# Performance work log

Measured on AMD Instinct MI355X. Metric: run time of the kernel, lower is better.

The kernel has to match this reference:

```python
import jax, jax.numpy as jnp
import numpy as np

EPS = 1e-6  # torch.nn.PairwiseDistance default eps: dist = ||x - y + eps||_2


def setup_inputs() -> dict:
    key = jax.random.key(0)
    k1, k2 = jax.random.split(key)
    samples = jax.random.normal(k1, (4096, 128), dtype=jnp.float32)   # batch of observations
    V = jax.random.uniform(k2, (65536, 128), dtype=jnp.float32)       # grown node codebook (torch.rand init)
    return {"samples": samples, "V": V}


def reference(samples, V):
    # activate_bmu, vectorized over the batch.
    # torch PairwiseDistance(p=2): d_n = || x - V_n + eps ||_2
    D = samples.shape[-1]
    x_sq = jnp.sum(samples * samples, axis=-1)        # [B]
    v_sq = jnp.sum(V * V, axis=-1)                    # [N]
    xv = jnp.einsum('bd,nd->bn', samples, V)          # [B, N]
    x_sum = jnp.sum(samples, axis=-1)                 # [B]
    v_sum = jnp.sum(V, axis=-1)                       # [N]
    sq = (x_sq[:, None] + v_sq[None, :] - 2.0 * xv
          + 2.0 * EPS * (x_sum[:, None] - v_sum[None, :]) + D * EPS * EPS)
    dists = jnp.sqrt(jnp.maximum(sq, 0.0))            # [B, N]
    # top-2 smallest distances -> BMU b, second BMU s
    neg_top2, idx = jax.lax.top_k(-dists, 2)          # [B, 2]
    b = idx[:, 0]
    s = idx[:, 1]
    a = jnp.exp(neg_top2[:, 0])                       # exp(-b_dist)
    return (b, s, a)
```

## Files before the change

### kernel.cpp

```cpp
#include <hip/hip_runtime.h>
#include <math.h>

#define NS 4096
#define NV 65536
#define DDIM 128
#define EPSV 1e-6f
#define NCHUNK 16
#define TILES_PER_CHUNK 32
#define FLTMAX 3.402823466e+38f
#define IMAX 0x7fffffff

#define VSQ_F   0
#define VSUM_F  65536
#define XSQ_F   131072
#define XSUM_F  135168
#define PART_F  139264
#define WS_TILED_BYTE 1605632
#define TILE_BYTES 65536
#define TILE_STRIDE 66560

typedef __attribute__((ext_vector_type(8)))  __bf16        bf16x8;
typedef __attribute__((ext_vector_type(8)))  unsigned short ush8;
typedef __attribute__((ext_vector_type(4)))  unsigned short ush4;
typedef __attribute__((ext_vector_type(16))) float          f32x16;

typedef const __attribute__((address_space(1))) unsigned int* gp_t;
typedef __attribute__((address_space(3))) unsigned int*       lp_t;

__device__ __forceinline__ void async_cp16(const void* g, void* l) {
    __builtin_amdgcn_global_load_lds((gp_t)g, (lp_t)l, 16, 0, 0);
}

__device__ __forceinline__ unsigned short f2bf(float x) {
    unsigned u = __builtin_bit_cast(unsigned, x);
    u += 0x7FFFu + ((u >> 16) & 1u);
    return (unsigned short)(u >> 16);
}
__device__ __forceinline__ float bf2f(unsigned short h) {
    unsigned u = ((unsigned)h) << 16;
    return __builtin_bit_cast(float, u);
}

__device__ __forceinline__ void merge2t(float& d1, int& i1, float& d2, int& i2,
                                        float d, int i) {
    bool b1 = (d < d1) || (d == d1 && i < i1);
    bool b2 = (d < d2) || (d == d2 && i < i2);
    if (b1) { d2 = d1; i2 = i1; d1 = d; i1 = i; }
    else if (b2) { d2 = d; i2 = i; }
}

__global__ void vq_precompute(const float* __restrict__ samples,
                              const float* __restrict__ V,
                              float* __restrict__ ws) {
    const int wave = threadIdx.x >> 6;
    const int lane = threadIdx.x & 63;
    int row = blockIdx.x * 4 + wave;
    const float* src; float* sqo; float* sumo; int r;
    if (row < NV) {
        r = row; src = V + (size_t)r * DDIM; sqo = ws + VSQ_F; sumo = ws + VSUM_F;
    } else {
        r = row - NV;
        if (r >= NS) return;
        src = samples + (size_t)r * DDIM; sqo = ws + XSQ_F; sumo = ws + XSUM_F;
    }
    float2 v = ((const float2*)src)[lane];
    float s = v.x + v.y;
    float q = v.x * v.x + v.y * v.y;
    #pragma unroll
    for (int off = 32; off >= 1; off >>= 1) {
        s += __shfl_xor(s, off);
        q += __shfl_xor(q, off);
    }
    if (lane == 0) { sqo[r] = q; sumo[r] = s; }
}

__global__ void vq_cj(const float* __restrict__ ws_f, char* __restrict__ ws) {
    int c = blockIdx.x * 256 + threadIdx.x;
    float cj = ws_f[VSQ_F + c] - 2.0f * EPSV * ws_f[VSUM_F + c];
    int tile = c >> 7, m = c & 127;
    *(float*)(ws + WS_TILED_BYTE + (size_t)tile * TILE_STRIDE + TILE_BYTES + m * 4) = cj;
}

__global__ void vq_convertV(const float* __restrict__ V, char* __restrict__ ws) {
    const int tile = blockIdx.x;
    const int tid = threadIdx.x;
    char* dst = ws + WS_TILED_BYTE + (size_t)tile * TILE_STRIDE;
    const float4* v4 = (const float4*)V;
    #pragma unroll
    for (int i = 0; i < 16; i++) {
        int flat = i * 256 + tid;
        int row = flat >> 5;
        int kq  = flat & 31;
        float4 g = v4[(size_t)(tile * 128 + row) * 32 + kq];
        int k0 = kq * 4;
        int s = k0 >> 4, q = (k0 >> 3) & 1, j0 = k0 & 7;
        float xs[4] = {g.x, g.y, g.z, g.w};
        ush4 h, l;
        #pragma unroll
        for (int e = 0; e < 4; e++) {
            unsigned short hh = f2bf(xs[e]);
            h[e] = hh;
            l[e] = f2bf(xs[e] - bf2f(hh));
        }
        *(ush4*)(dst + ((((s * 2 + 0) * 2 + q) * 128) + row) * 16 + j0 * 2) = h;
        *(ush4*)(dst + ((((s * 2 + 1) * 2 + q) * 128) + row) * 16 + j0 * 2) = l;
    }
}

__global__ __launch_bounds__(256, 2)
void vq_gemm_topk(const float* __restrict__ samples, char* __restrict__ ws) {
    __shared__ __align__(16) char lds[TILE_STRIDE];
    const int tid = threadIdx.x;
    const int w = tid >> 6, lane = tid & 63;
    const int l31 = lane & 31, q = lane >> 5;
    const int st = blockIdx.x;
    const int chunk = blockIdx.y;
    const int nrow = st * 128 + w * 32 + l31;

    ush8 bh[8], bl[8];
    const float4* s4 = (const float4*)samples;
    #pragma unroll
    for (int s = 0; s < 8; s++) {
        float4 x0 = s4[(size_t)nrow * 32 + s * 4 + q * 2];
        float4 x1 = s4[(size_t)nrow * 32 + s * 4 + q * 2 + 1];
        float xs[8] = {x0.x, x0.y, x0.z, x0.w, x1.x, x1.y, x1.z, x1.w};
        #pragma unroll
        for (int j = 0; j < 8; j++) {
            float y = -2.0f * xs[j];
            unsigned short hh = f2bf(y);
            bh[s][j] = hh;
            bl[s][j] = f2bf(y - bf2f(hh));
        }
    }

    float d1 = FLTMAX, d2 = FLTMAX;
    int i1 = IMAX, i2 = IMAX;

    const char* tile0 = ws + WS_TILED_BYTE + (size_t)(chunk * TILES_PER_CHUNK) * TILE_STRIDE;

    for (int it = 0; it < TILES_PER_CHUNK; it++) {
        const char* src = tile0 + (size_t)it * TILE_STRIDE;
        #pragma unroll
        for (int i = 0; i < 16; i++) {
            int off = (i * 256 + tid) * 16;
            async_cp16(src + off, lds + off);
        }
        if (tid < 64) {
            int off = TILE_BYTES + tid * 16;
            async_cp16(src + off, lds + off);
        }
        __syncthreads();

        f32x16 acc[4];
        #pragma unroll
        for (int mi = 0; mi < 4; mi++)
            #pragma unroll
            for (int r = 0; r < 16; r++) acc[mi][r] = 0.0f;

        #pragma unroll
        for (int s = 0; s < 8; s++) {
            bf16x8 bhs = __builtin_bit_cast(bf16x8, bh[s]);
            bf16x8 bls = __builtin_bit_cast(bf16x8, bl[s]);
            #pragma unroll
            for (int mi = 0; mi < 4; mi++) {
                bf16x8 ah = *(const bf16x8*)(lds + (size_t)((((s * 2 + 0) * 2 + q) * 128) + mi * 32 + l31) * 16);
                bf16x8 al = *(const bf16x8*)(lds + (size_t)((((s * 2 + 1) * 2 + q) * 128) + mi * 32 + l31) * 16);
                acc[mi] = __builtin_amdgcn_mfma_f32_32x32x16_bf16(ah, bhs, acc[mi], 0, 0, 0);
                acc[mi] = __builtin_amdgcn_mfma_f32_32x32x16_bf16(ah, bls, acc[mi], 0, 0, 0);
                acc[mi] = __builtin_amdgcn_mfma_f32_32x32x16_bf16(al, bhs, acc[mi], 0, 0, 0);
            }
        }

        const int cbase = chunk * 4096 + it * 128 + 4 * q;
        #pragma unroll
        for (int mi = 0; mi < 4; mi++) {
            #pragma unroll
            for (int g = 0; g < 4; g++) {
                float4 cj = *(const float4*)(lds + TILE_BYTES + (size_t)(mi * 32 + g * 8 + 4 * q) * 4);
                float cje[4] = {cj.x, cj.y, cj.z, cj.w};
                #pragma unroll
                for (int e = 0; e < 4; e++) {
                    float v = acc[mi][g * 4 + e] + cje[e];
                    int idx = cbase + mi * 32 + g * 8 + e;
                    bool c1 = v < d1, c2 = v < d2;
                    float nd2 = c1 ? d1 : v;
                    int   ni2 = c1 ? i1 : idx;
                    d2 = c2 ? nd2 : d2;
                    i2 = c2 ? ni2 : i2;
                    d1 = c1 ? v : d1;
                    i1 = c1 ? idx : i1;
                }
            }
        }
        __syncthreads();
    }

    {
        float od1 = __shfl_xor(d1, 32), od2 = __shfl_xor(d2, 32);
        int   oi1 = __shfl_xor(i1, 32), oi2 = __shfl_xor(i2, 32);
        merge2t(d1, i1, d2, i2, od1, oi1);
        merge2t(d1, i1, d2, i2, od2, oi2);
    }
    if (q == 0) {
        int sample = st * 128 + w * 32 + l31;
        float4* part = (float4*)( (float*)((char*)ws) + PART_F );
        part[(size_t)sample * NCHUNK + chunk] = make_float4(d1, d2, (float)i1, (float)i2);
    }
}

__global__ void vq_reduce(const float* __restrict__ ws_f, float* __restrict__ out) {
    int m = blockIdx.x * 256 + threadIdx.x;
    if (m >= NS) return;
    const float4* part = (const float4*)(ws_f + PART_F);
    float d1 = FLTMAX, d2 = FLTMAX;
    int i1 = IMAX, i2 = IMAX;
    for (int c = 0; c < NCHUNK; c++) {
        float4 p = part[(size_t)m * NCHUNK + c];
        merge2t(d1, i1, d2, i2, p.x, (int)p.z);
        merge2t(d1, i1, d2, i2, p.y, (int)p.w);
    }
    float ci = ws_f[XSQ_F + m] + 2.0f * EPSV * ws_f[XSUM_F + m] + (float)DDIM * EPSV * EPSV;
    float sq = fmaxf(ci + d1, 0.0f);
    out[m]          = (float)i1;
    out[NS + m]     = (float)i2;
    out[2 * NS + m] = expf(-sqrtf(sq));
}

extern "C" void kernel_launch(void* const* d_in, const int* in_sizes, int n_in,
                              void* d_out, int out_size, void* d_ws, size_t ws_size,
                              hipStream_t stream) {
    (void)in_sizes; (void)n_in; (void)out_size; (void)ws_size;
    const float* samples = (const float*)d_in[0];
    const float* V = (const float*)d_in[1];
    float* out = (float*)d_out;
    float* ws_f = (float*)d_ws;
    char*  ws_b = (char*)d_ws;

    vq_precompute<<<dim3((NV + NS) / 4), 256, 0, stream>>>(samples, V, ws_f);
    vq_cj<<<dim3(NV / 256), 256, 0, stream>>>(ws_f, ws_b);
    vq_convertV<<<dim3(NV / 128), 256, 0, stream>>>(V, ws_b);
    vq_gemm_topk<<<dim3(NS / 128, NCHUNK), 256, 0, stream>>>(samples, ws_b);
    vq_reduce<<<dim3(NS / 256), 256, 0, stream>>>(ws_f, out);
}
```

Baseline: 297.8 us.

## Track top-2 values only in main GEMM, recover indices in a sparse second pass

The main GEMM loop now keeps only per-row top-2 distance values with cheap min/max ops, dropping per-element index tracking. The column bias cj is folded into the accumulator init. A merge kernel buckets samples by the chunks that hold their winners, and a recovery kernel recomputes only those chunks to find the matching indices with atomicMin. Preprocessing kernels are fused into a single prep kernel. Recomputation has to reproduce the exact float values for the equality checks to hit, and the extra launches and recompute passes add cost.

```diff
diff --git a/kernel.cpp b/kernel.cpp
--- a/kernel.cpp
+++ b/kernel.cpp
@@ -10,11 +10,14 @@
 #define FLTMAX 3.402823466e+38f
 #define IMAX 0x7fffffff
 
-#define VSQ_F   0
-#define VSUM_F  65536
-#define XSQ_F   131072
-#define XSUM_F  135168
-#define PART_F  139264
+#define XSQ_F    0
+#define XSUM_F   4096
+#define PART_F   8192
+#define D12_F    139264
+#define CNT_I    147456
+#define CELL1_I  147472
+#define CELL2_I  151568
+#define BUCKET_I 155664
 #define WS_TILED_BYTE 1605632
 #define TILE_BYTES 65536
 #define TILE_STRIDE 66560
@@ -41,59 +44,106 @@
     return __builtin_bit_cast(float, u);
 }
 
-__device__ __forceinline__ void merge2t(float& d1, int& i1, float& d2, int& i2,
-                                        float d, int i) {
-    bool b1 = (d < d1) || (d == d1 && i < i1);
-    bool b2 = (d < d2) || (d == d2 && i < i2);
-    if (b1) { d2 = d1; i2 = i1; d1 = d; i1 = i; }
-    else if (b2) { d2 = d; i2 = i; }
-}
-
-__global__ void vq_precompute(const float* __restrict__ samples,
-                              const float* __restrict__ V,
-                              float* __restrict__ ws) {
-    const int wave = threadIdx.x >> 6;
-    const int lane = threadIdx.x & 63;
-    int row = blockIdx.x * 4 + wave;
-    const float* src; float* sqo; float* sumo; int r;
-    if (row < NV) {
-        r = row; src = V + (size_t)r * DDIM; sqo = ws + VSQ_F; sumo = ws + VSUM_F;
-    } else {
-        r = row - NV;
-        if (r >= NS) return;
-        src = samples + (size_t)r * DDIM; sqo = ws + XSQ_F; sumo = ws + XSUM_F;
-    }
-    float2 v = ((const float2*)src)[lane];
-    float s = v.x + v.y;
-    float q = v.x * v.x + v.y * v.y;
-    #pragma unroll
-    for (int off = 32; off >= 1; off >>= 1) {
-        s += __shfl_xor(s, off);
-        q += __shfl_xor(q, off);
-    }
-    if (lane == 0) { sqo[r] = q; sumo[r] = s; }
-}
-
-__global__ void vq_cj(const float* __restrict__ ws_f, char* __restrict__ ws) {
-    int c = blockIdx.x * 256 + threadIdx.x;
-    float cj = ws_f[VSQ_F + c] - 2.0f * EPSV * ws_f[VSUM_F + c];
-    int tile = c >> 7, m = c & 127;
-    *(float*)(ws + WS_TILED_BYTE + (size_t)tile * TILE_STRIDE + TILE_BYTES + m * 4) = cj;
-}
-
-__global__ void vq_convertV(const float* __restrict__ V, char* __restrict__ ws) {
-    const int tile = blockIdx.x;
+__device__ __forceinline__ void stage_tile(const char* src, char* lds, int tid) {
+    #pragma unroll
+    for (int i = 0; i < 16; i++) {
+        int off = (i * 256 + tid) * 16;
+        async_cp16(src + off, lds + off);
+    }
+    if (tid < 64) {
+        int off = TILE_BYTES + tid * 16;
+        async_cp16(src + off, lds + off);
+    }
+}
+
+__device__ __forceinline__ void load_bfrag(const float* __restrict__ samples,
+                                           int srow, int q, ush8* bh, ush8* bl) {
+    const float4* s4 = (const float4*)samples;
+    #pragma unroll
+    for (int s = 0; s < 8; s++) {
+        float4 x0 = s4[(size_t)srow * 32 + s * 4 + q * 2];
+        float4 x1 = s4[(size_t)srow * 32 + s * 4 + q * 2 + 1];
+        float xs[8] = {x0.x, x0.y, x0.z, x0.w, x1.x, x1.y, x1.z, x1.w};
+        #pragma unroll
+        for (int j = 0; j < 8; j++) {
+            float y = -2.0f * xs[j];
+            unsigned short hh = f2bf(y);
+            bh[s][j] = hh;
+            bl[s][j] = f2bf(y - bf2f(hh));
+        }
+    }
+}
+
+__device__ __forceinline__ void tile_mfma(const char* lds, const ush8* bh, const ush8* bl,
+                                          int q, int l31, f32x16 acc[4]) {
+    #pragma unroll
+    for (int mi = 0; mi < 4; mi++) {
+        #pragma unroll
+        for (int g = 0; g < 4; g++) {
+            float4 cj = *(const float4*)(lds + TILE_BYTES + (size_t)(mi * 32 + g * 8 + 4 * q) * 4);
+            acc[mi][g * 4 + 0] = cj.x;
+            acc[mi][g * 4 + 1] = cj.y;
+            acc[mi][g * 4 + 2] = cj.z;
+            acc[mi][g * 4 + 3] = cj.w;
+        }
+    }
+    #pragma unroll
+    for (int s = 0; s < 8; s++) {
+        bf16x8 bhs = __builtin_bit_cast(bf16x8, bh[s]);
+        bf16x8 bls = __builtin_bit_cast(bf16x8, bl[s]);
+        #pragma unroll
+        for (int mi = 0; mi < 4; mi++) {
+            bf16x8 ah = *(const bf16x8*)(lds + (size_t)((((s * 2 + 0) * 2 + q) * 128) + mi * 32 + l31) * 16);
+            bf16x8 al = *(const bf16x8*)(lds + (size_t)((((s * 2 + 1) * 2 + q) * 128) + mi * 32 + l31) * 16);
+            acc[mi] = __builtin_amdgcn_mfma_f32_32x32x16_bf16(ah, bhs, acc[mi], 0, 0, 0);
+            acc[mi] = __builtin_amdgcn_mfma_f32_32x32x16_bf16(ah, bls, acc[mi], 0, 0, 0);
+            acc[mi] = __builtin_amdgcn_mfma_f32_32x32x16_bf16(al, bhs, acc[mi], 0, 0, 0);
+        }
+    }
+}
+
+__global__ void vq_prep(const float* __restrict__ samples,
+                        const float* __restrict__ V,
+                        char* __restrict__ ws) {
+    float* ws_f = (float*)ws;
+    int* ws_i = (int*)ws;
+    const int b = blockIdx.x;
     const int tid = threadIdx.x;
+    if (b >= NV / 128) {
+        if (b == NV / 128 && tid < NCHUNK) ws_i[CNT_I + tid] = 0;
+        int row = (b - NV / 128) * 4 + (tid >> 6);
+        int lane = tid & 63;
+        float2 v = ((const float2*)(samples + (size_t)row * DDIM))[lane];
+        float s = v.x + v.y;
+        float q = v.x * v.x + v.y * v.y;
+        #pragma unroll
+        for (int off = 32; off >= 1; off >>= 1) {
+            s += __shfl_xor(s, off);
+            q += __shfl_xor(q, off);
+        }
+        if (lane == 0) { ws_f[XSQ_F + row] = q; ws_f[XSUM_F + row] = s; }
+        return;
+    }
+    const int tile = b;
     char* dst = ws + WS_TILED_BYTE + (size_t)tile * TILE_STRIDE;
     const float4* v4 = (const float4*)V;
     #pragma unroll
     for (int i = 0; i < 16; i++) {
         int flat = i * 256 + tid;
         int row = flat >> 5;
-        int kq  = flat & 31;
+        int kq = flat & 31;
         float4 g = v4[(size_t)(tile * 128 + row) * 32 + kq];
+        float s = g.x + g.y + g.z + g.w;
+        float q2 = g.x * g.x + g.y * g.y + g.z * g.z + g.w * g.w;
+        #pragma unroll
+        for (int off = 16; off >= 1; off >>= 1) {
+            s += __shfl_xor(s, off);
+            q2 += __shfl_xor(q2, off);
+        }
+        if ((tid & 31) == 0)
+            *(float*)(dst + TILE_BYTES + row * 4) = q2 - 2.0f * EPSV * s;
         int k0 = kq * 4;
-        int s = k0 >> 4, q = (k0 >> 3) & 1, j0 = k0 & 7;
+        int sI = k0 >> 4, qI = (k0 >> 3) & 1, j0 = k0 & 7;
         float xs[4] = {g.x, g.y, g.z, g.w};
         ush4 h, l;
         #pragma unroll
@@ -102,8 +152,8 @@
             h[e] = hh;
             l[e] = f2bf(xs[e] - bf2f(hh));
         }
-        *(ush4*)(dst + ((((s * 2 + 0) * 2 + q) * 128) + row) * 16 + j0 * 2) = h;
-        *(ush4*)(dst + ((((s * 2 + 1) * 2 + q) * 128) + row) * 16 + j0 * 2) = l;
+        *(ush4*)(dst + ((((sI * 2 + 0) * 2 + qI) * 128) + row) * 16 + j0 * 2) = h;
+        *(ush4*)(dst + ((((sI * 2 + 1) * 2 + qI) * 128) + row) * 16 + j0 * 2) = l;
     }
 }
 
@@ -118,112 +168,146 @@
     const int nrow = st * 128 + w * 32 + l31;
 
     ush8 bh[8], bl[8];
-    const float4* s4 = (const float4*)samples;
-    #pragma unroll
-    for (int s = 0; s < 8; s++) {
-        float4 x0 = s4[(size_t)nrow * 32 + s * 4 + q * 2];
-        float4 x1 = s4[(size_t)nrow * 32 + s * 4 + q * 2 + 1];
-        float xs[8] = {x0.x, x0.y, x0.z, x0.w, x1.x, x1.y, x1.z, x1.w};
-        #pragma unroll
-        for (int j = 0; j < 8; j++) {
-            float y = -2.0f * xs[j];
-            unsigned short hh = f2bf(y);
-            bh[s][j] = hh;
-            bl[s][j] = f2bf(y - bf2f(hh));
-        }
-    }
-
-    float d1 = FLTMAX, d2 = FLTMAX;
-    int i1 = IMAX, i2 = IMAX;
+    load_bfrag(samples, nrow, q, bh, bl);
+
+    float rd1[4], rd2[4];
+    #pragma unroll
+    for (int mi = 0; mi < 4; mi++) { rd1[mi] = FLTMAX; rd2[mi] = FLTMAX; }
 
     const char* tile0 = ws + WS_TILED_BYTE + (size_t)(chunk * TILES_PER_CHUNK) * TILE_STRIDE;
 
     for (int it = 0; it < TILES_PER_CHUNK; it++) {
-        const char* src = tile0 + (size_t)it * TILE_STRIDE;
-        #pragma unroll
-        for (int i = 0; i < 16; i++) {
-            int off = (i * 256 + tid) * 16;
-            async_cp16(src + off, lds + off);
-        }
-        if (tid < 64) {
-            int off = TILE_BYTES + tid * 16;
-            async_cp16(src + off, lds + off);
-        }
+        stage_tile(tile0 + (size_t)it * TILE_STRIDE, lds, tid);
         __syncthreads();
-
         f32x16 acc[4];
-        #pragma unroll
-        for (int mi = 0; mi < 4; mi++)
+        tile_mfma(lds, bh, bl, q, l31, acc);
+        #pragma unroll
+        for (int mi = 0; mi < 4; mi++) {
             #pragma unroll
-            for (int r = 0; r < 16; r++) acc[mi][r] = 0.0f;
-
-        #pragma unroll
-        for (int s = 0; s < 8; s++) {
-            bf16x8 bhs = __builtin_bit_cast(bf16x8, bh[s]);
-            bf16x8 bls = __builtin_bit_cast(bf16x8, bl[s]);
+            for (int r = 0; r < 16; r++) {
+                float v = acc[mi][r];
+                rd2[mi] = fminf(rd2[mi], fmaxf(rd1[mi], v));
+                rd1[mi] = fminf(rd1[mi], v);
+            }
+        }
+        __syncthreads();
+    }
+
+    float d1 = rd1[0], d2 = rd2[0];
+    #pragma unroll
+    for (int mi = 1; mi < 4; mi++) {
+        float t = fmaxf(d1, rd1[mi]);
+        d1 = fminf(d1, rd1[mi]);
+        d2 = fminf(fminf(t, d2), rd2[mi]);
+    }
+    {
+        float od1 = __shfl_xor(d1, 32), od2 = __shfl_xor(d2, 32);
+        float t = fmaxf(d1, od1);
+        d1 = fminf(d1, od1);
+        d2 = fminf(fminf(t, d2), od2);
+    }
+    if (q == 0) {
+        float2* part = (float2*)((float*)ws + PART_F);
+        part[(size_t)nrow * NCHUNK + chunk] = make_float2(d1, d2);
+    }
+}
+
+__global__ void vq_merge(float* __restrict__ ws_f, float* __restrict__ out) {
+    const int m = blockIdx.x * 256 + threadIdx.x;
+    const int lane = threadIdx.x & 63;
+    int* ws_i = (int*)ws_f;
+    const float2* part = (const float2*)(ws_f + PART_F);
+    float2 p[NCHUNK];
+    float g1 = FLTMAX, g2 = FLTMAX;
+    #pragma unroll
+    for (int c = 0; c < NCHUNK; c++) {
+        p[c] = part[(size_t)m * NCHUNK + c];
+        float t = fmaxf(g1, p[c].x);
+        g1 = fminf(g1, p[c].x);
+        g2 = fminf(fminf(t, g2), p[c].y);
+    }
+    ((float2*)(ws_f + D12_F))[m] = make_float2(g1, g2);
+    ws_i[CELL1_I + m] = IMAX;
+    ws_i[CELL2_I + m] = IMAX;
+    float ci = ws_f[XSQ_F + m] + 2.0f * EPSV * ws_f[XSUM_F + m] + (float)DDIM * EPSV * EPSV;
+    out[2 * NS + m] = expf(-sqrtf(fmaxf(ci + g1, 0.0f)));
+    #pragma unroll
+    for (int c = 0; c < NCHUNK; c++) {
+        bool want = (p[c].x == g1) || (p[c].x == g2) || (p[c].y == g2);
+        unsigned long long mk = __ballot(want);
+        if (mk) {
+            int leader = (int)__ffsll(mk) - 1;
+            int base = 0;
+            if (lane == leader) base = atomicAdd(&ws_i[CNT_I + c], (int)__popcll(mk));
+            base = __shfl(base, leader);
+            if (want) {
+                int pos = base + (int)__popcll(mk & ((1ull << lane) - 1ull));
+                ws_i[BUCKET_I + c * NS + pos] = m;
+            }
+        }
+    }
+}
+
+__global__ __launch_bounds__(256, 2)
+void vq_recover(const float* __restrict__ samples, char* __restrict__ ws) {
+    __shared__ __align__(16) char lds[TILE_STRIDE];
+    const int tid = threadIdx.x;
+    const int w = tid >> 6, lane = tid & 63;
+    const int l31 = lane & 31, q = lane >> 5;
+    const int tg = blockIdx.x;
+    const int chunk = blockIdx.z;
+    int* ws_i = (int*)ws;
+    float* ws_f = (float*)ws;
+    const int cnt = ws_i[CNT_I + chunk];
+    const char* tile0 = ws + WS_TILED_BYTE + (size_t)(chunk * TILES_PER_CHUNK) * TILE_STRIDE;
+
+    for (int sy = blockIdx.y; sy * 128 < cnt; sy += 4) {
+        int slot = sy * 128 + w * 32 + l31;
+        bool valid = slot < cnt;
+        int sample = valid ? ws_i[BUCKET_I + chunk * NS + slot] : 0;
+        ush8 bh[8], bl[8];
+        load_bfrag(samples, sample, q, bh, bl);
+        float d1t, d2t;
+        if (valid) {
+            float2 dt = ((const float2*)(ws_f + D12_F))[sample];
+            d1t = dt.x; d2t = dt.y;
+        } else {
+            d1t = __int_as_float(0x7fc00000);
+            d2t = d1t;
+        }
+        #pragma unroll 1
+        for (int it = tg * 4; it < tg * 4 + 4; it++) {
+            stage_tile(tile0 + (size_t)it * TILE_STRIDE, lds, tid);
+            __syncthreads();
+            f32x16 acc[4];
+            tile_mfma(lds, bh, bl, q, l31, acc);
+            const int cbase = chunk * 4096 + it * 128 + 4 * q;
             #pragma unroll
             for (int mi = 0; mi < 4; mi++) {
-                bf16x8 ah = *(const bf16x8*)(lds + (size_t)((((s * 2 + 0) * 2 + q) * 128) + mi * 32 + l31) * 16);
-                bf16x8 al = *(const bf16x8*)(lds + (size_t)((((s * 2 + 1) * 2 + q) * 128) + mi * 32 + l31) * 16);
-                acc[mi] = __builtin_amdgcn_mfma_f32_32x32x16_bf16(ah, bhs, acc[mi], 0, 0, 0);
-                acc[mi] = __builtin_amdgcn_mfma_f32_32x32x16_bf16(ah, bls, acc[mi], 0, 0, 0);
-                acc[mi] = __builtin_amdgcn_mfma_f32_32x32x16_bf16(al, bhs, acc[mi], 0, 0, 0);
-            }
-        }
-
-        const int cbase = chunk * 4096 + it * 128 + 4 * q;
-        #pragma unroll
-        for (int mi = 0; mi < 4; mi++) {
-            #pragma unroll
-            for (int g = 0; g < 4; g++) {
-                float4 cj = *(const float4*)(lds + TILE_BYTES + (size_t)(mi * 32 + g * 8 + 4 * q) * 4);
-                float cje[4] = {cj.x, cj.y, cj.z, cj.w};
                 #pragma unroll
-                for (int e = 0; e < 4; e++) {
-                    float v = acc[mi][g * 4 + e] + cje[e];
-                    int idx = cbase + mi * 32 + g * 8 + e;
-                    bool c1 = v < d1, c2 = v < d2;
-                    float nd2 = c1 ? d1 : v;
-                    int   ni2 = c1 ? i1 : idx;
-                    d2 = c2 ? nd2 : d2;
-                    i2 = c2 ? ni2 : i2;
-                    d1 = c1 ? v : d1;
-                    i1 = c1 ? idx : i1;
+                for (int r = 0; r < 16; r++) {
+                    float v = acc[mi][r];
+                    if (v == d1t) {
+                        int idx = cbase + mi * 32 + (r >> 2) * 8 + (r & 3);
+                        int old = atomicMin(&ws_i[CELL1_I + sample], idx);
+                        int loser = old > idx ? old : idx;
+                        atomicMin(&ws_i[CELL2_I + sample], loser);
+                    } else if (v == d2t) {
+                        int idx = cbase + mi * 32 + (r >> 2) * 8 + (r & 3);
+                        atomicMin(&ws_i[CELL2_I + sample], idx);
+                    }
                 }
             }
-        }
-        __syncthreads();
-    }
-
-    {
-        float od1 = __shfl_xor(d1, 32), od2 = __shfl_xor(d2, 32);
-        int   oi1 = __shfl_xor(i1, 32), oi2 = __shfl_xor(i2, 32);
-        merge2t(d1, i1, d2, i2, od1, oi1);
-        merge2t(d1, i1, d2, i2, od2, oi2);
-    }
-    if (q == 0) {
-        int sample = st * 128 + w * 32 + l31;
-        float4* part = (float4*)( (float*)((char*)ws) + PART_F );
-        part[(size_t)sample * NCHUNK + chunk] = make_float4(d1, d2, (float)i1, (float)i2);
-    }
-}
-
-__global__ void vq_reduce(const float* __restrict__ ws_f, float* __restrict__ out) {
-    int m = blockIdx.x * 256 + threadIdx.x;
-    if (m >= NS) return;
-    const float4* part = (const float4*)(ws_f + PART_F);
-    float d1 = FLTMAX, d2 = FLTMAX;
-    int i1 = IMAX, i2 = IMAX;
-    for (int c = 0; c < NCHUNK; c++) {
-        float4 p = part[(size_t)m * NCHUNK + c];
-        merge2t(d1, i1, d2, i2, p.x, (int)p.z);
-        merge2t(d1, i1, d2, i2, p.y, (int)p.w);
-    }
-    float ci = ws_f[XSQ_F + m] + 2.0f * EPSV * ws_f[XSUM_F + m] + (float)DDIM * EPSV * EPSV;
-    float sq = fmaxf(ci + d1, 0.0f);
-    out[m]          = (float)i1;
-    out[NS + m]     = (float)i2;
-    out[2 * NS + m] = expf(-sqrtf(sq));
+            __syncthreads();
+        }
+    }
+}
+
+__global__ void vq_finalize(const char* __restrict__ ws, float* __restrict__ out) {
+    const int m = blockIdx.x * 256 + threadIdx.x;
+    const int* ws_i = (const int*)ws;
+    out[m]      = (float)ws_i[CELL1_I + m];
+    out[NS + m] = (float)ws_i[CELL2_I + m];
 }
 
 extern "C" void kernel_launch(void* const* d_in, const int* in_sizes, int n_in,
@@ -236,9 +320,9 @@
     float* ws_f = (float*)d_ws;
     char*  ws_b = (char*)d_ws;
 
-    vq_precompute<<<dim3((NV + NS) / 4), 256, 0, stream>>>(samples, V, ws_f);
-    vq_cj<<<dim3(NV / 256), 256, 0, stream>>>(ws_f, ws_b);
-    vq_convertV<<<dim3(NV / 128), 256, 0, stream>>>(V, ws_b);
+    vq_prep<<<dim3(NV / 128 + NS / 4), 256, 0, stream>>>(samples, V, ws_b);
     vq_gemm_topk<<<dim3(NS / 128, NCHUNK), 256, 0, stream>>>(samples, ws_b);
-    vq_reduce<<<dim3(NS / 256), 256, 0, stream>>>(ws_f, out);
-}
+    vq_merge<<<dim3(NS / 256), 256, 0, stream>>>(ws_f, out);
+    vq_recover<<<dim3(8, 4, NCHUNK), 256, 0, stream>>>(samples, ws_b);
+    vq_finalize<<<dim3(NS / 256), 256, 0, stream>>>(ws_b, out);
+}
```

After: 341.9 us. +14.8%, slower.
